# Kernel tuning notes

Measured on AMD Instinct MI355X. Metric: run time of the kernel, lower is better.

## Reference

```python
import jax, jax.numpy as jnp
import numpy as np
from jax import lax

B, DIM, RES = 1024, 384, 7
HEADS, KEY_DIM, ATTN_RATIO = 8, 32, 4
N = RES * RES            # 49
KH = KEY_DIM * HEADS     # 256
D = ATTN_RATIO * KEY_DIM # 128
DH = D * HEADS           # 1024
SCALE = KEY_DIM ** -0.5


def _rel_pos_idx():
    ii, jj = np.meshgrid(np.arange(RES), np.arange(RES), indexing='ij')
    pos = np.stack([ii.ravel(), jj.ravel()])          # [2, N]
    rel = np.abs(pos[:, :, None] - pos[:, None, :])   # [2, N, N]
    return jnp.asarray(rel[0] * RES + rel[1])         # [N, N] int

REL_IDX = _rel_pos_idx()


def conv1x1_bn(x, w, b, s, o):
    # 1x1 conv (pointwise GEMM) + eval-mode BatchNorm folded to scale/shift
    y = jnp.einsum('oc,bchw->bohw', w, x) + b[:, None, None]
    return y * s[:, None, None] + o[:, None, None]


def setup_inputs() -> dict:
    key = jax.random.key(0)
    ks = jax.random.split(key, 32)
    f = lambda i, shape, scale=0.02: jax.random.normal(ks[i], shape, jnp.float32) * scale
    u = lambda i, shape: jax.random.uniform(ks[i], shape, jnp.float32, 0.5, 1.5)
    inp = {
        'x': jax.random.normal(ks[0], (B, DIM, RES, RES), jnp.float32),
        'q_w': f(1, (KH, DIM)), 'q_b': f(2, (KH,)), 'q_s': u(3, (KH,)), 'q_o': f(4, (KH,)),
        'k_w': f(5, (KH, DIM)), 'k_b': f(6, (KH,)), 'k_s': u(7, (KH,)), 'k_o': f(8, (KH,)),
        'v_w': f(9, (DH, DIM)), 'v_b': f(10, (DH,)), 'v_s': u(11, (DH,)), 'v_o': f(12, (DH,)),
        'vl_w': f(13, (DH, 1, 3, 3)), 'vl_b': f(14, (DH,)), 'vl_s': u(15, (DH,)), 'vl_o': f(16, (DH,)),
        'th1_w': f(17, (HEADS, HEADS), 0.1), 'th1_b': f(18, (HEADS,)),
        'th2_w': f(19, (HEADS, HEADS), 0.1), 'th2_b': f(20, (HEADS,)),
        'p_w': f(21, (DIM, DH)), 'p_b': f(22, (DIM,)), 'p_s': u(23, (DIM,)), 'p_o': f(24, (DIM,)),
        'ab': f(25, (HEADS, N), 0.1),
    }
    return inp


def reference(x, q_w, q_b, q_s, q_o, k_w, k_b, k_s, k_o, v_w, v_b, v_s, v_o,
              vl_w, vl_b, vl_s, vl_o, th1_w, th1_b, th2_w, th2_b,
              p_w, p_b, p_s, p_o, ab):
    b = x.shape[0]
    q = conv1x1_bn(x, q_w, q_b, q_s, q_o).reshape(b, HEADS, KEY_DIM, N)
    q = q.transpose(0, 1, 3, 2)                         # [B,H,N,kd]
    k = conv1x1_bn(x, k_w, k_b, k_s, k_o).reshape(b, HEADS, KEY_DIM, N)  # [B,H,kd,N]
    v4 = conv1x1_bn(x, v_w, v_b, v_s, v_o)              # [B,DH,7,7]
    # local depthwise 3x3 branch + BN
    vl = lax.conv_general_dilated(v4, vl_w, (1, 1), 'SAME',
                                  feature_group_count=DH,
                                  dimension_numbers=('NCHW', 'OIHW', 'NCHW'))
    vl = (vl + vl_b[:, None, None]) * vl_s[:, None, None] + vl_o[:, None, None]
    v = v4.reshape(b, HEADS, D, N).transpose(0, 1, 3, 2)  # [B,H,N,d]

    bias = ab[:, REL_IDX]                                # [H,N,N]
    attn = jnp.einsum('bhnd,bhdm->bhnm', q, k) * SCALE + bias[None]
    # talking head 1 (1x1 conv over head dim)
    attn = jnp.einsum('ij,bjnm->binm', th1_w, attn) + th1_b[None, :, None, None]
    attn = jax.nn.softmax(attn, axis=-1)
    # talking head 2
    attn = jnp.einsum('ij,bjnm->binm', th2_w, attn) + th2_b[None, :, None, None]

    out = jnp.einsum('bhnm,bhmd->bhnd', attn, v)         # [B,H,N,d]
    out = out.transpose(0, 1, 3, 2).reshape(b, DH, RES, RES) + vl
    out = jax.nn.gelu(out, approximate=False)            # nn.GELU default = exact
    out = conv1x1_bn(out, p_w, p_b, p_s, p_o)            # [B,DIM,7,7]
    return out
```

## Files before the change

kernel.cpp:

```cpp
#include <hip/hip_runtime.h>
#include <math.h>

typedef unsigned short u16;
typedef unsigned int u32;
typedef short short8 __attribute__((ext_vector_type(8)));
typedef float f32x4 __attribute__((ext_vector_type(4)));
typedef unsigned int u32x2 __attribute__((ext_vector_type(2)));

#define SCALE_QK 0.17677669529663687f
#define POFF 26880

__device__ __forceinline__ float b2f(u16 v) { return __uint_as_float(((u32)v) << 16); }
__device__ __forceinline__ u16 f2b(float f) {
  u32 u = __float_as_uint(f);
  return (u16)((u + 0x7fffu + ((u >> 16) & 1u)) >> 16);
}

__device__ __forceinline__ float gelu_f(float z) {
  float y = z * 0.70710678118654752f;
  float a = fabsf(y);
  float t = __builtin_amdgcn_rcpf(fmaf(0.3275911f, a, 1.0f));
  float e = __expf(-y * y);
  float p = fmaf(1.061405429f, t, -1.453152027f);
  p = fmaf(p, t, 1.421413741f);
  p = fmaf(p, t, -0.284496736f);
  p = fmaf(p, t, 0.254829592f);
  p = p * t * e;
  float phi = (y >= 0.f) ? fmaf(-0.5f, p, 1.0f) : 0.5f * p;
  return z * phi;
}

__global__ __launch_bounds__(256) void k_pre(
    const float* __restrict__ th1w, const float* __restrict__ th1b, const float* __restrict__ ab,
    const float* __restrict__ qb, const float* __restrict__ qs, const float* __restrict__ qo,
    const float* __restrict__ kb, const float* __restrict__ ks, const float* __restrict__ ko,
    const float* __restrict__ vb, const float* __restrict__ vs, const float* __restrict__ vo,
    const float* __restrict__ pb, const float* __restrict__ ps, const float* __restrict__ po,
    const float* __restrict__ qw, const float* __restrict__ kw,
    const float* __restrict__ vw, const float* __restrict__ pw,
    float* __restrict__ bias2, float* __restrict__ alpha, float* __restrict__ beta,
    float* __restrict__ alphap, float* __restrict__ betap,
    u16* __restrict__ Wqk, u16* __restrict__ Wv, u16* __restrict__ Wp)
{
  int gid = blockIdx.x * 256 + threadIdx.x;
  if (gid < 19208) {
    int i = gid / 2401, rem = gid % 2401, n = rem / 49, m = rem % 49;
    int ry = abs(n / 7 - m / 7), rx = abs(n % 7 - m % 7);
    int idx = ry * 7 + rx;
    float acc = th1b[i];
    #pragma unroll
    for (int j = 0; j < 8; j++) acc += th1w[i * 8 + j] * ab[j * 49 + idx];
    bias2[gid] = acc;
  } else if (gid < 20744) {
    int c = gid - 19208;
    const float *s, *bb, *oo; int idx;
    if (c < 256)      { s = qs; bb = qb; oo = qo; idx = c; }
    else if (c < 512) { s = ks; bb = kb; oo = ko; idx = c - 256; }
    else              { s = vs; bb = vb; oo = vo; idx = c - 512; }
    float sv = s[idx];
    alpha[c] = sv;
    beta[c] = sv * bb[idx] + oo[idx];
  } else if (gid < 21128) {
    int c = gid - 20744;
    float sv = ps[c];
    alphap[c] = sv;
    betap[c] = sv * pb[c] + po[c];
  } else {
    int g = gid - 21128;
    if (g < 98304)       Wqk[g] = f2b(qw[g]);
    else if (g < 196608) Wqk[g] = f2b(kw[g - 98304]);
    else if (g < 589824) Wv[g - 196608] = f2b(vw[g - 196608]);
    else if (g < 983040) Wp[g - 589824] = f2b(pw[g - 589824]);
  }
}

__global__ __launch_bounds__(512, 4) void k_qk(
    const float* __restrict__ x, const u16* __restrict__ Wqk,
    const float* __restrict__ alpha, const float* __restrict__ beta,
    u16* __restrict__ Zs)
{
  __shared__ __align__(16) u16 lds[37376];
  u16* XT = lds;
  u16* Tq = lds + 26112;
  u16* Tk = lds + 31744;
  int t = threadIdx.x, wv = t >> 6, l = t & 63, quad = l >> 4, l16 = l & 15;
  int b = blockIdx.x;
  const float* xb = x + (size_t)b * 18816;

  for (int e = t; e < 18816; e += 512) {
    int k = e / 49, n = e - k * 49;
    XT[n * 408 + k] = f2b(xb[e]);
  }
  for (int e = t; e < 3060; e += 512) {
    int r = e / 204, kk = e - r * 204;
    ((u32*)(XT + (49 + r) * 408))[kk] = 0;
  }
  __syncthreads();

  u16* Pg = Zs + (size_t)b * 50176 + POFF;
  int isK = wv >= 4, wl = wv & 3;
  for (int hp = 0; hp < 4; hp++) {
    int cbase = (isK ? 256 : 0) + hp * 64 + wl * 16;
    f32x4 acc[4] = {};
    const u16* Wr = Wqk + (size_t)(cbase + l16) * 384;
    short8 afr[12];
    #pragma unroll
    for (int ks = 0; ks < 12; ks++) afr[ks] = *(const short8*)(Wr + ks * 32 + quad * 8);
    #pragma unroll
    for (int ks = 0; ks < 12; ks++) {
      #pragma unroll
      for (int nt = 0; nt < 4; nt++) {
        short8 bf = *(const short8*)(&XT[(nt * 16 + l16) * 408 + ks * 32 + quad * 8]);
        acc[nt] = __builtin_amdgcn_mfma_f32_16x16x32_bf16(afr[ks], bf, acc[nt], 0, 0, 0);
      }
    }
    u16* Tdst = isK ? Tk : Tq;
    #pragma unroll
    for (int reg = 0; reg < 4; reg++) {
      int c = cbase + quad * 4 + reg;
      float al = alpha[c], be = beta[c];
      int cl = wl * 16 + quad * 4 + reg;
      #pragma unroll
      for (int nt = 0; nt < 4; nt++)
        Tdst[(nt * 16 + l16) * 88 + cl] = f2b(acc[nt][reg] * al + be);
    }
    __syncthreads();
    #pragma unroll
    for (int ui = 0; ui < 4; ui++) {
      int u = wv * 4 + ui;
      int hl = u >> 4, tn = (u >> 2) & 3, tm = u & 3;
      short8 a  = *(const short8*)(&Tq[(tn * 16 + l16) * 88 + hl * 32 + quad * 8]);
      short8 bb = *(const short8*)(&Tk[(tm * 16 + l16) * 88 + hl * 32 + quad * 8]);
      f32x4 c = {};
      c = __builtin_amdgcn_mfma_f32_16x16x32_bf16(a, bb, c, 0, 0, 0);
      int h = hp * 2 + hl;
      #pragma unroll
      for (int r = 0; r < 4; r++) {
        int n = tn * 16 + quad * 4 + r, m = tm * 16 + l16;
        if (n < 49 && m < 49) Pg[(h * 52 + n) * 56 + m] = f2b(c[r] * SCALE_QK);
      }
    }
    __syncthreads();
  }
}

__global__ __launch_bounds__(256, 4) void k_mix(
    u16* __restrict__ Zs, const float* __restrict__ bias2,
    const float* __restrict__ th1w, const float* __restrict__ th1b,
    const float* __restrict__ th2w, const float* __restrict__ th2b)
{
  __shared__ u16 SB[23296];
  __shared__ float TH[144];
  int t = threadIdx.x, b = blockIdx.x;
  u32* Pg32 = (u32*)(Zs + (size_t)b * 50176 + POFF);
  for (int e = t; e < 11648; e += 256) ((u32*)SB)[e] = Pg32[e];
  if (t < 64)       TH[t] = th1w[t];
  else if (t < 72)  TH[t] = th1b[t - 64];
  else if (t < 136) TH[t] = th2w[t - 72];
  else if (t < 144) TH[t] = th2b[t - 136];
  __syncthreads();
  for (int e = t; e < 2401; e += 256) {
    int n = e / 49, m = e - n * 49;
    float s[8], uo[8];
    #pragma unroll
    for (int j = 0; j < 8; j++) s[j] = b2f(SB[(j * 52 + n) * 56 + m]);
    #pragma unroll
    for (int i = 0; i < 8; i++) {
      float a2 = bias2[(i * 49 + n) * 49 + m];
      #pragma unroll
      for (int j = 0; j < 8; j++) a2 += TH[i * 8 + j] * s[j];
      uo[i] = a2;
    }
    #pragma unroll
    for (int i = 0; i < 8; i++) SB[(i * 52 + n) * 56 + m] = f2b(uo[i]);
  }
  __syncthreads();
  for (int r0 = t; r0 < 392; r0 += 256) {
    int i = r0 / 49, n = r0 - i * 49;
    u16* row = &SB[(i * 52 + n) * 56];
    float v[49]; float mx = -1e30f;
    #pragma unroll
    for (int m = 0; m < 49; m++) { v[m] = b2f(row[m]); mx = fmaxf(mx, v[m]); }
    float sum = 0.f;
    #pragma unroll
    for (int m = 0; m < 49; m++) { v[m] = __expf(v[m] - mx); sum += v[m]; }
    float inv = 1.f / sum;
    #pragma unroll
    for (int m = 0; m < 49; m++) row[m] = f2b(v[m] * inv);
  }
  __syncthreads();
  for (int e = t; e < 2401; e += 256) {
    int n = e / 49, m = e - n * 49;
    float s[8], uo[8];
    #pragma unroll
    for (int j = 0; j < 8; j++) s[j] = b2f(SB[(j * 52 + n) * 56 + m]);
    #pragma unroll
    for (int i = 0; i < 8; i++) {
      float a2 = TH[136 + i];
      #pragma unroll
      for (int j = 0; j < 8; j++) a2 += TH[72 + i * 8 + j] * s[j];
      uo[i] = a2;
    }
    #pragma unroll
    for (int i = 0; i < 8; i++) SB[(i * 52 + n) * 56 + m] = f2b(uo[i]);
  }
  __syncthreads();
  for (int e = t; e < 11648; e += 256) Pg32[e] = ((u32*)SB)[e];
}

__global__ __launch_bounds__(512, 4) void k_av(
    const float* __restrict__ x, const u16* __restrict__ Wv,
    const float* __restrict__ alpha, const float* __restrict__ beta,
    const float* __restrict__ vlw, const float* __restrict__ vlb,
    const float* __restrict__ vls, const float* __restrict__ vlo,
    u16* __restrict__ Zs)
{
  __shared__ __align__(16) u16 lds[38968];
  u16* XT = lds;
  u16* VT = lds + 26112;
  u16* Ph = lds + 35328;
  int t = threadIdx.x, wv = t >> 6, l = t & 63, quad = l >> 4, l16 = l & 15;
  int b = blockIdx.x;
  const float* xb = x + (size_t)b * 18816;

  for (int e = t; e < 18816; e += 512) {
    int k = e / 49, n = e - k * 49;
    XT[n * 408 + k] = f2b(xb[e]);
  }
  for (int e = t; e < 3060; e += 512) {
    int r = e / 204, kk = e - r * 204;
    ((u32*)(XT + (49 + r) * 408))[kk] = 0;
  }
  for (int e = t; e < 4608; e += 512) ((u32*)VT)[e] = 0;
  __syncthreads();

  u16* Zb = Zs + (size_t)b * 50176;
  const u16* Pgb = Zb + POFF;
  for (int h = 0; h < 8; h++) {
    {
      const u32* src = (const u32*)(Pgb + h * 2912);
      for (int e = t; e < 1456; e += 512) ((u32*)Ph)[e] = src[e];
    }
    const u16* Wr = Wv + (size_t)(h * 128 + wv * 16 + l16) * 384;
    short8 afr[12];
    #pragma unroll
    for (int ks = 0; ks < 12; ks++) afr[ks] = *(const short8*)(Wr + ks * 32 + quad * 8);
    int d = wv * 16 + l16, c = h * 128 + d;
    float w9[9];
    #pragma unroll
    for (int j = 0; j < 9; j++) w9[j] = vlw[c * 9 + j];
    float sv = vls[c];
    float cb = sv * vlb[c] + vlo[c];

    f32x4 va[4] = {};
    #pragma unroll
    for (int ks = 0; ks < 12; ks++) {
      #pragma unroll
      for (int nt = 0; nt < 4; nt++) {
        short8 bf = *(const short8*)(&XT[(nt * 16 + l16) * 408 + ks * 32 + quad * 8]);
        va[nt] = __builtin_amdgcn_mfma_f32_16x16x32_bf16(afr[ks], bf, va[nt], 0, 0, 0);
      }
    }
    #pragma unroll
    for (int reg = 0; reg < 4; reg++) {
      int dl = wv * 16 + quad * 4 + reg;
      int cc = h * 128 + dl;
      float al = alpha[512 + cc], be = beta[512 + cc];
      #pragma unroll
      for (int nt = 0; nt < 4; nt++) {
        int m = nt * 16 + l16;
        if (m < 49) VT[dl * 72 + 8 + m] = f2b(va[nt][reg] * al + be);
      }
    }
    __syncthreads();
    f32x4 oa[4] = {};
    #pragma unroll
    for (int ks2 = 0; ks2 < 2; ks2++) {
      int mb = ks2 * 32 + quad * 8;
      short8 bf = *(const short8*)(&VT[(wv * 16 + l16) * 72 + 8 + mb]);
      #pragma unroll
      for (int tn = 0; tn < 4; tn++) {
        short8 af = *(const short8*)(&Ph[(tn * 16 + l16) * 56 + mb]);
        oa[tn] = __builtin_amdgcn_mfma_f32_16x16x32_bf16(af, bf, oa[tn], 0, 0, 0);
      }
    }
    const u16* vtr = &VT[d * 72];
    #pragma unroll
    for (int tn = 0; tn < 4; tn++) {
      int n0 = tn * 16 + quad * 4;
      const u16* vr = vtr + n0;
      float q[20];
      #pragma unroll
      for (int jj = 0; jj < 5; jj++) {
        u32x2 U = *(const u32x2*)(vr + jj * 4);
        q[jj * 4 + 0] = __uint_as_float(U.x << 16);
        q[jj * 4 + 1] = __uint_as_float(U.x & 0xffff0000u);
        q[jj * 4 + 2] = __uint_as_float(U.y << 16);
        q[jj * 4 + 3] = __uint_as_float(U.y & 0xffff0000u);
      }
      #pragma unroll
      for (int r = 0; r < 4; r++) {
        int n = n0 + r;
        int yi = (n * 37) >> 8;
        int xi = n - yi * 7;
        bool xl = xi > 0, xr = xi < 6;
        float w0m = xl ? w9[0] : 0.f, w3m = xl ? w9[3] : 0.f, w6m = xl ? w9[6] : 0.f;
        float w2m = xr ? w9[2] : 0.f, w5m = xr ? w9[5] : 0.f, w8m = xr ? w9[8] : 0.f;
        float conv = q[r]      * w0m + q[r + 1]  * w9[1] + q[r + 2]  * w2m
                   + q[r + 7]  * w3m + q[r + 8]  * w9[4] + q[r + 9]  * w5m
                   + q[r + 14] * w6m + q[r + 15] * w9[7] + q[r + 16] * w8m;
        float z = oa[tn][r] + conv * sv + cb;
        float g = gelu_f(z);
        if (tn < 3 || n < 49) Zb[(size_t)c * 49 + n] = f2b(g);
      }
    }
    __syncthreads();
  }
}

__global__ __launch_bounds__(512, 4) void k_proj(
    const u16* __restrict__ Wp, const u16* __restrict__ Zs,
    const float* __restrict__ alphap, const float* __restrict__ betap,
    float* __restrict__ out)
{
  __shared__ u16 Bs[128 * 152];
  int t = threadIdx.x, wv = t >> 6, l = t & 63, quad = l >> 4, l16 = l & 15;
  int mb = blockIdx.x % 3;
  size_t b0 = (size_t)(blockIdx.x / 3) * 2;
  f32x4 acc[8] = {};
  const u16* Wr = Wp + (size_t)(mb * 128 + wv * 16 + l16) * 1024;
  for (int k0 = 0; k0 < 1024; k0 += 128) {
    for (int e = t; e < 16384; e += 512) {
      int np = e & 127, kk = e >> 7;
      int pb = np >> 6, n = np & 63;
      u16 v = 0;
      if (n < 49) v = Zs[(b0 + pb) * 50176 + (size_t)(k0 + kk) * 49 + n];
      Bs[np * 152 + kk] = v;
    }
    __syncthreads();
    #pragma unroll
    for (int ksi = 0; ksi < 4; ksi++) {
      short8 af = *(const short8*)(Wr + k0 + ksi * 32 + quad * 8);
      #pragma unroll
      for (int nt = 0; nt < 8; nt++) {
        short8 bf = *(const short8*)(&Bs[(nt * 16 + l16) * 152 + ksi * 32 + quad * 8]);
        acc[nt] = __builtin_amdgcn_mfma_f32_16x16x32_bf16(af, bf, acc[nt], 0, 0, 0);
      }
    }
    __syncthreads();
  }
  #pragma unroll
  for (int reg = 0; reg < 4; reg++) {
    int c = mb * 128 + wv * 16 + quad * 4 + reg;
    float al = alphap[c], be = betap[c];
    #pragma unroll
    for (int nt = 0; nt < 8; nt++) {
      int np = nt * 16 + l16, pb = np >> 6, n = np & 63;
      if (n < 49) out[(b0 + pb) * 18816 + (size_t)c * 49 + n] = acc[nt][reg] * al + be;
    }
  }
}

extern "C" void kernel_launch(void* const* d_in, const int* in_sizes, int n_in,
                              void* d_out, int out_size, void* d_ws, size_t ws_size,
                              hipStream_t stream) {
  const float* x    = (const float*)d_in[0];
  const float* qw   = (const float*)d_in[1];
  const float* qb   = (const float*)d_in[2];
  const float* qs   = (const float*)d_in[3];
  const float* qo   = (const float*)d_in[4];
  const float* kw   = (const float*)d_in[5];
  const float* kb   = (const float*)d_in[6];
  const float* ks   = (const float*)d_in[7];
  const float* ko   = (const float*)d_in[8];
  const float* vw   = (const float*)d_in[9];
  const float* vb   = (const float*)d_in[10];
  const float* vs   = (const float*)d_in[11];
  const float* vo   = (const float*)d_in[12];
  const float* vlw  = (const float*)d_in[13];
  const float* vlb  = (const float*)d_in[14];
  const float* vls  = (const float*)d_in[15];
  const float* vlo  = (const float*)d_in[16];
  const float* th1w = (const float*)d_in[17];
  const float* th1b = (const float*)d_in[18];
  const float* th2w = (const float*)d_in[19];
  const float* th2b = (const float*)d_in[20];
  const float* pw   = (const float*)d_in[21];
  const float* pb   = (const float*)d_in[22];
  const float* ps   = (const float*)d_in[23];
  const float* po   = (const float*)d_in[24];
  const float* ab   = (const float*)d_in[25];
  float* out = (float*)d_out;
  char* ws = (char*)d_ws;

  float* bias2  = (float*)(ws + 0);
  float* alpha  = (float*)(ws + 77056);
  float* beta   = (float*)(ws + 83200);
  float* alphap = (float*)(ws + 89344);
  float* betap  = (float*)(ws + 90880);
  u16*   Wqk16  = (u16*)(ws + 92416);
  u16*   Wv16   = (u16*)(ws + 485632);
  u16*   Wp16   = (u16*)(ws + 1272064);
  u16*   Zs     = (u16*)(ws + 2058496);

  k_pre<<<3923, 256, 0, stream>>>(th1w, th1b, ab, qb, qs, qo, kb, ks, ko,
                                  vb, vs, vo, pb, ps, po, qw, kw, vw, pw,
                                  bias2, alpha, beta, alphap, betap,
                                  Wqk16, Wv16, Wp16);
  k_qk<<<1024, 512, 0, stream>>>(x, Wqk16, alpha, beta, Zs);
  k_mix<<<1024, 256, 0, stream>>>(Zs, bias2, th1w, th1b, th2w, th2b);
  k_av<<<1024, 512, 0, stream>>>(x, Wv16, alpha, beta, vlw, vlb, vls, vlo, Zs);
  k_proj<<<1536, 512, 0, stream>>>(Wp16, Zs, alphap, betap, out);
}
```

Baseline: 651.0 us.

## Store GELU output token-major and vectorize projection loads, move attention buffer to output

The attention-probability slab moves out of the Zs workspace into the output buffer, so k_av no longer overwrites the slab it reads when it writes Z. With that conflict gone, Z is stored as [n][channel], letting k_proj fill LDS with 16-byte vector loads instead of scalar strided gathers. k_qk now zero-fills the padding of the P slab explicitly. k_proj also remaps block order so neighbouring blocks share weight tiles. The trade-off is that k_av's Z stores become strided across channels.

Result: faster. 575.7 us (-11.6%).

```diff
diff --git a/kernel.cpp b/kernel.cpp
--- a/kernel.cpp
+++ b/kernel.cpp
@@ -8,7 +8,7 @@
 typedef unsigned int u32x2 __attribute__((ext_vector_type(2)));
 
 #define SCALE_QK 0.17677669529663687f
-#define POFF 26880
+#define PSLAB 23296
 
 __device__ __forceinline__ float b2f(u16 v) { return __uint_as_float(((u32)v) << 16); }
 __device__ __forceinline__ u16 f2b(float f) {
@@ -77,7 +77,7 @@
 __global__ __launch_bounds__(512, 4) void k_qk(
     const float* __restrict__ x, const u16* __restrict__ Wqk,
     const float* __restrict__ alpha, const float* __restrict__ beta,
-    u16* __restrict__ Zs)
+    u16* __restrict__ Pbuf)
 {
   __shared__ __align__(16) u16 lds[37376];
   u16* XT = lds;
@@ -97,7 +97,7 @@
   }
   __syncthreads();
 
-  u16* Pg = Zs + (size_t)b * 50176 + POFF;
+  u16* Pg = Pbuf + (size_t)b * PSLAB;
   int isK = wv >= 4, wl = wv & 3;
   for (int hp = 0; hp < 4; hp++) {
     int cbase = (isK ? 256 : 0) + hp * 64 + wl * 16;
@@ -137,7 +137,8 @@
       #pragma unroll
       for (int r = 0; r < 4; r++) {
         int n = tn * 16 + quad * 4 + r, m = tm * 16 + l16;
-        if (n < 49 && m < 49) Pg[(h * 52 + n) * 56 + m] = f2b(c[r] * SCALE_QK);
+        if (n < 52 && m < 56)
+          Pg[(h * 52 + n) * 56 + m] = (n < 49 && m < 49) ? f2b(c[r] * SCALE_QK) : (u16)0;
       }
     }
     __syncthreads();
@@ -145,14 +146,14 @@
 }
 
 __global__ __launch_bounds__(256, 4) void k_mix(
-    u16* __restrict__ Zs, const float* __restrict__ bias2,
+    u16* __restrict__ Pbuf, const float* __restrict__ bias2,
     const float* __restrict__ th1w, const float* __restrict__ th1b,
     const float* __restrict__ th2w, const float* __restrict__ th2b)
 {
   __shared__ u16 SB[23296];
   __shared__ float TH[144];
   int t = threadIdx.x, b = blockIdx.x;
-  u32* Pg32 = (u32*)(Zs + (size_t)b * 50176 + POFF);
+  u32* Pg32 = (u32*)(Pbuf + (size_t)b * PSLAB);
   for (int e = t; e < 11648; e += 256) ((u32*)SB)[e] = Pg32[e];
   if (t < 64)       TH[t] = th1w[t];
   else if (t < 72)  TH[t] = th1b[t - 64];
@@ -213,7 +214,7 @@
     const float* __restrict__ alpha, const float* __restrict__ beta,
     const float* __restrict__ vlw, const float* __restrict__ vlb,
     const float* __restrict__ vls, const float* __restrict__ vlo,
-    u16* __restrict__ Zs)
+    const u16* __restrict__ Pbuf, u16* __restrict__ Zs)
 {
   __shared__ __align__(16) u16 lds[38968];
   u16* XT = lds;
@@ -235,7 +236,7 @@
   __syncthreads();
 
   u16* Zb = Zs + (size_t)b * 50176;
-  const u16* Pgb = Zb + POFF;
+  const u16* Pgb = Pbuf + (size_t)b * PSLAB;
   for (int h = 0; h < 8; h++) {
     {
       const u32* src = (const u32*)(Pgb + h * 2912);
@@ -311,7 +312,7 @@
                    + q[r + 14] * w6m + q[r + 15] * w9[7] + q[r + 16] * w8m;
         float z = oa[tn][r] + conv * sv + cb;
         float g = gelu_f(z);
-        if (tn < 3 || n < 49) Zb[(size_t)c * 49 + n] = f2b(g);
+        if (n < 49) Zb[(size_t)n * 1024 + c] = f2b(g);
       }
     }
     __syncthreads();
@@ -319,23 +320,28 @@
 }
 
 __global__ __launch_bounds__(512, 4) void k_proj(
-    const u16* __restrict__ Wp, const u16* __restrict__ Zs,
+    const u16* __restrict__ Wp, const u16* __restrict__ Zt,
     const float* __restrict__ alphap, const float* __restrict__ betap,
     float* __restrict__ out)
 {
-  __shared__ u16 Bs[128 * 152];
+  __shared__ __align__(16) u16 Bs[128 * 152];
   int t = threadIdx.x, wv = t >> 6, l = t & 63, quad = l >> 4, l16 = l & 15;
-  int mb = blockIdx.x % 3;
-  size_t b0 = (size_t)(blockIdx.x / 3) * 2;
+  int g = blockIdx.x;
+  int vb = (g & 7) * 192 + (g >> 3);
+  int mb = vb % 3;
+  size_t b0 = (size_t)(vb / 3) * 2;
   f32x4 acc[8] = {};
   const u16* Wr = Wp + (size_t)(mb * 128 + wv * 16 + l16) * 1024;
   for (int k0 = 0; k0 < 1024; k0 += 128) {
-    for (int e = t; e < 16384; e += 512) {
-      int np = e & 127, kk = e >> 7;
+    #pragma unroll
+    for (int i = 0; i < 4; i++) {
+      int ch = t + i * 512;
+      int np = ch >> 4, ck = ch & 15;
       int pb = np >> 6, n = np & 63;
-      u16 v = 0;
-      if (n < 49) v = Zs[(b0 + pb) * 50176 + (size_t)(k0 + kk) * 49 + n];
-      Bs[np * 152 + kk] = v;
+      short8 v = {};
+      if (n < 49)
+        v = *(const short8*)(Zt + (b0 + pb) * 50176 + (size_t)n * 1024 + k0 + ck * 8);
+      *(short8*)(&Bs[np * 152 + ck * 8]) = v;
     }
     __syncthreads();
     #pragma unroll
@@ -393,6 +399,8 @@
   float* out = (float*)d_out;
   char* ws = (char*)d_ws;
 
+  u16* Pbuf = (u16*)d_out;
+
   float* bias2  = (float*)(ws + 0);
   float* alpha  = (float*)(ws + 77056);
   float* beta   = (float*)(ws + 83200);
@@ -407,8 +415,8 @@
                                   vb, vs, vo, pb, ps, po, qw, kw, vw, pw,
                                   bias2, alpha, beta, alphap, betap,
                                   Wqk16, Wv16, Wp16);
-  k_qk<<<1024, 512, 0, stream>>>(x, Wqk16, alpha, beta, Zs);
-  k_mix<<<1024, 256, 0, stream>>>(Zs, bias2, th1w, th1b, th2w, th2b);
-  k_av<<<1024, 512, 0, stream>>>(x, Wv16, alpha, beta, vlw, vlb, vls, vlo, Zs);
+  k_qk<<<1024, 512, 0, stream>>>(x, Wqk16, alpha, beta, Pbuf);
+  k_mix<<<1024, 256, 0, stream>>>(Pbuf, bias2, th1w, th1b, th2w, th2b);
+  k_av<<<1024, 512, 0, stream>>>(x, Wv16, alpha, beta, vlw, vlb, vls, vlo, Pbuf, Zs);
   k_proj<<<1536, 512, 0, stream>>>(Wp16, Zs, alphap, betap, out);
 }
```
